# Optimization experiments

Measured on AMD Instinct MI355X. Metric: run time of the kernel, lower is better.

## Reference

```python
import jax, jax.numpy as jnp
import numpy as np


def _layernorm(x, g, b, eps=1e-5):
    mu = jnp.mean(x, axis=-1, keepdims=True)
    var = jnp.mean((x - mu) ** 2, axis=-1, keepdims=True)
    return g * (x - mu) * jax.lax.rsqrt(var + eps) + b


def _pos_encoding(S, D, dtype):
    # standard sinusoidal positional encoding [S, D]
    pos = jnp.arange(S, dtype=jnp.float32)[:, None]
    i = jnp.arange(0, D, 2, dtype=jnp.float32)[None, :]
    ang = pos / jnp.power(10000.0, i / D)
    return jnp.stack([jnp.sin(ang), jnp.cos(ang)], axis=-1).reshape(S, D).astype(dtype)


def _mha(x, theta, Wc, bc, num_heads):
    # Quantum projection: per-wire RX(x)+RX(theta) from |0>, <Z> = cos(x+theta).
    # The module uses ONE shared q_layer for q, k, v, so q == k == v.
    B, S, D = x.shape
    dk = D // num_heads
    p = jnp.cos(x + theta)                                    # [B,S,D]
    ph = p.reshape(B, S, num_heads, dk)                        # [B,S,H,dk]
    scale = 1.0 / jnp.sqrt(jnp.asarray(dk, x.dtype))
    scores = jnp.einsum('bqhd,bkhd->bhqk', ph, ph) * scale     # [B,H,S,S]
    attn = jax.nn.softmax(scores, axis=-1)
    out = jnp.einsum('bhqk,bkhd->bqhd', attn, ph).reshape(B, S, D)
    return out @ Wc + bc


def _ffn(x, theta, W1, b1, W2, b2):
    # RY-encoder + trainable RY per wire -> <Z> = cos(x + theta)
    h = jnp.cos(x + theta)
    h = h @ W1 + b1
    return jax.nn.relu(h) @ W2 + b2


def _forward(tokens, embedding, theta_attn, Wc, bc, ln1_g, ln1_b, theta_ffn,
             W1, b1, W2, b2, ln2_g, ln2_b, Wcls, bcls, num_heads):
    x = embedding[tokens]                                      # [B,S,D]
    B, S, D = x.shape
    x = x + _pos_encoding(S, D, x.dtype)
    n_blocks = theta_attn.shape[0]
    for l in range(n_blocks):  # small fixed layer count
        a = _mha(x, theta_attn[l], Wc[l], bc[l], num_heads)
        x = _layernorm(x + a, ln1_g[l], ln1_b[l])
        f = _ffn(x, theta_ffn[l], W1[l], b1[l], W2[l], b2[l])
        x = _layernorm(x + f, ln2_g[l], ln2_b[l])
    pooled = jnp.mean(x, axis=1)                               # [B,D]
    return pooled @ Wcls + bcls                                # [B,C]


def setup_inputs() -> dict:
    key = jax.random.key(0)
    ks = jax.random.split(key, 8)
    V, D, L, F, C = 32000, 512, 2, 2048, 10
    B, S = 8, 1024
    s = 0.02
    return {
        'tokens': jax.random.randint(ks[0], (B, S), 0, V, dtype=jnp.int32),
        'embedding': jax.random.normal(ks[1], (V, D), jnp.float32) * s,
        'theta_attn': jax.random.normal(ks[2], (L, D), jnp.float32) * s,
        'Wc': jax.random.normal(ks[3], (L, D, D), jnp.float32) * s,
        'bc': jnp.zeros((L, D), jnp.float32),
        'ln1_g': jnp.ones((L, D), jnp.float32),
        'ln1_b': jnp.zeros((L, D), jnp.float32),
        'theta_ffn': jax.random.normal(ks[4], (L, D), jnp.float32) * s,
        'W1': jax.random.normal(ks[5], (L, D, F), jnp.float32) * s,
        'b1': jnp.zeros((L, F), jnp.float32),
        'W2': jax.random.normal(ks[6], (L, F, D), jnp.float32) * s,
        'b2': jnp.zeros((L, D), jnp.float32),
        'ln2_g': jnp.ones((L, D), jnp.float32),
        'ln2_b': jnp.zeros((L, D), jnp.float32),
        'Wcls': jax.random.normal(ks[7], (D, C), jnp.float32) * s,
        'bcls': jnp.zeros((C,), jnp.float32),
        'num_heads': 8,
    }


def reference(tokens, embedding, theta_attn, Wc, bc, ln1_g, ln1_b, theta_ffn,
              W1, b1, W2, b2, ln2_g, ln2_b, Wcls, bcls, num_heads):
    return _forward(tokens, embedding, theta_attn, Wc, bc, ln1_g, ln1_b,
                    theta_ffn, W1, b1, W2, b2, ln2_g, ln2_b, Wcls, bcls, num_heads)
```

## Files before the change

### kernel.cpp

```cpp
#include <hip/hip_runtime.h>
#include <math.h>

#define BB 8
#define SS 1024
#define DD 512
#define HH 8
#define DK 64
#define FF 2048
#define NCLS 10
#define ROWS (BB*SS)
#define NLAYERS 2

typedef short bf16x8 __attribute__((ext_vector_type(8)));
typedef float f32x4 __attribute__((ext_vector_type(4)));

__device__ inline short f2bf(float f) {
    unsigned u = __float_as_uint(f);
    u += 0x7FFF + ((u >> 16) & 1);
    return (short)(u >> 16);
}

__device__ inline void gload_lds16(const void* g, void* l) {
    __builtin_amdgcn_global_load_lds((const __attribute__((address_space(1))) void*)g,
                                     (__attribute__((address_space(3))) void*)l, 16, 0, 0);
}

__global__ __launch_bounds__(128) void k_embed_pe(const int* __restrict__ tokens,
                                                  const float* __restrict__ emb,
                                                  float* __restrict__ x) {
    int row = blockIdx.x;
    int s = row & (SS - 1);
    int tok = tokens[row];
    const float4* e = reinterpret_cast<const float4*>(emb + (size_t)tok * DD);
    float4 v = e[threadIdx.x];
    float pe[4];
#pragma unroll
    for (int j = 0; j < 4; ++j) {
        int d = threadIdx.x * 4 + j;
        int jj = d >> 1;
        float inv = expf(-((float)(2 * jj) / (float)DD) * 9.210340371976184f);
        float ang = (float)s * inv;
        pe[j] = (d & 1) ? cosf(ang) : sinf(ang);
    }
    v.x += pe[0]; v.y += pe[1]; v.z += pe[2]; v.w += pe[3];
    reinterpret_cast<float4*>(x + (size_t)row * DD)[threadIdx.x] = v;
}

template <int WT>
__global__ __launch_bounds__(256) void k_cosp(const float* __restrict__ x,
                                              const float* __restrict__ theta,
                                              short* __restrict__ p,
                                              short* __restrict__ pt) {
    int d0 = blockIdx.x * 64, s0 = blockIdx.y * 64, b = blockIdx.z;
    int t = threadIdx.x;
    int tc = t & 15, tr = t >> 4;
    __shared__ short lt[64][68];
    float4 th = *reinterpret_cast<const float4*>(theta + d0 + tc * 4);
#pragma unroll
    for (int i = 0; i < 4; ++i) {
        int s = tr + 16 * i;
        float4 xv = *reinterpret_cast<const float4*>(
            x + ((size_t)b * SS + s0 + s) * DD + d0 + tc * 4);
        short4 o;
        o.x = f2bf(cosf(xv.x + th.x));
        o.y = f2bf(cosf(xv.y + th.y));
        o.z = f2bf(cosf(xv.z + th.z));
        o.w = f2bf(cosf(xv.w + th.w));
        *reinterpret_cast<short4*>(p + ((size_t)b * SS + s0 + s) * DD + d0 + tc * 4) = o;
        if (WT) {
            lt[tc * 4 + 0][s] = o.x;
            lt[tc * 4 + 1][s] = o.y;
            lt[tc * 4 + 2][s] = o.z;
            lt[tc * 4 + 3][s] = o.w;
        }
    }
    if (WT) {
        __syncthreads();
#pragma unroll
        for (int i = 0; i < 4; ++i) {
            int d = tr + 16 * i;
            short4 v;
            v.x = lt[d][tc * 4 + 0];
            v.y = lt[d][tc * 4 + 1];
            v.z = lt[d][tc * 4 + 2];
            v.w = lt[d][tc * 4 + 3];
            *reinterpret_cast<short4*>(pt + ((size_t)b * DD + d0 + d) * SS + s0 + tc * 4) = v;
        }
    }
}

__global__ __launch_bounds__(256) void k_wtrans(const float* __restrict__ W,
                                                short* __restrict__ Wt,
                                                int K, int N) {
    __shared__ float tile[32][33];
    int n0 = blockIdx.x * 32, k0 = blockIdx.y * 32;
    int tx = threadIdx.x & 31, ty = threadIdx.x >> 5;
#pragma unroll
    for (int i = 0; i < 4; ++i)
        tile[ty + 8 * i][tx] = W[(size_t)(k0 + ty + 8 * i) * N + n0 + tx];
    __syncthreads();
#pragma unroll
    for (int i = 0; i < 4; ++i)
        Wt[(size_t)(n0 + ty + 8 * i) * K + k0 + tx] = f2bf(tile[tx][ty + 8 * i]);
}

__global__ __launch_bounds__(256) void k_attn(const short* __restrict__ p,
                                              const short* __restrict__ pt,
                                              short* __restrict__ aout) {
    int qc = blockIdx.x, h = blockIdx.y, b = blockIdx.z;
    int t = threadIdx.x, w = t >> 6, l = t & 63;
    int lg = l >> 4, lr = l & 15;

    __shared__ __attribute__((aligned(16))) short Kt[128 * 64];
    __shared__ __attribute__((aligned(16))) short Vt[64 * 128];
    __shared__ __attribute__((aligned(16))) short Pl[4][16 * 136];

    const size_t prow = ((size_t)b * SS + qc * 64 + w * 16 + lr) * DD + h * DK;
    bf16x8 qf0 = *reinterpret_cast<const bf16x8*>(p + prow + lg * 8);
    bf16x8 qf1 = *reinterpret_cast<const bf16x8*>(p + prow + 32 + lg * 8);

    f32x4 acc[4];
#pragma unroll
    for (int dt = 0; dt < 4; ++dt) acc[dt] = (f32x4){0.f, 0.f, 0.f, 0.f};
    float denom = 0.f;

    const short* pK = p + (size_t)b * SS * DD + h * DK;
    const short* pV = pt + ((size_t)b * DD + h * DK) * SS;

    short* myP = &Pl[w][0];

    for (int k0 = 0; k0 < SS; k0 += 128) {
        __syncthreads();
#pragma unroll
        for (int i = 0; i < 4; ++i) {
            int c = i * 256 + t;
            int row = c >> 3, sl = c & 7, ssl = sl ^ (row & 7);
            gload_lds16(pK + (size_t)(k0 + row) * DD + ssl * 8,
                        Kt + (size_t)(i * 256 + w * 64) * 8);
        }
#pragma unroll
        for (int i = 0; i < 4; ++i) {
            int c = i * 256 + t;
            int row = c >> 4, sl = c & 15, ssl = sl ^ ((row & 7) * 2);
            gload_lds16(pV + (size_t)row * SS + k0 + ssl * 8,
                        Vt + (size_t)(i * 256 + w * 64) * 8);
        }
        asm volatile("s_waitcnt vmcnt(0)" ::: "memory");
        __syncthreads();

        f32x4 sc[8];
#pragma unroll
        for (int kt = 0; kt < 8; ++kt) {
            int row = kt * 16 + lr;
            bf16x8 ka0 = *reinterpret_cast<const bf16x8*>(Kt + row * 64 + ((lg ^ (row & 7)) * 8));
            bf16x8 ka1 = *reinterpret_cast<const bf16x8*>(Kt + row * 64 + (((lg + 4) ^ (row & 7)) * 8));
            f32x4 z = (f32x4){0.f, 0.f, 0.f, 0.f};
            z = __builtin_amdgcn_mfma_f32_16x16x32_bf16(ka0, qf0, z, 0, 0, 0);
            z = __builtin_amdgcn_mfma_f32_16x16x32_bf16(ka1, qf1, z, 0, 0, 0);
            sc[kt] = z;
        }
#pragma unroll
        for (int kt = 0; kt < 8; ++kt) {
            float e0 = __expf(sc[kt].x * 0.125f);
            float e1 = __expf(sc[kt].y * 0.125f);
            float e2 = __expf(sc[kt].z * 0.125f);
            float e3 = __expf(sc[kt].w * 0.125f);
            denom += (e0 + e1) + (e2 + e3);
            short4 pk;
            pk.x = f2bf(e0); pk.y = f2bf(e1); pk.z = f2bf(e2); pk.w = f2bf(e3);
            *reinterpret_cast<short4*>(myP + lr * 136 + kt * 16 + lg * 4) = pk;
        }
        asm volatile("s_waitcnt lgkmcnt(0)" ::: "memory");
#pragma unroll
        for (int kt2 = 0; kt2 < 4; ++kt2) {
            bf16x8 pb = *reinterpret_cast<const bf16x8*>(myP + lr * 136 + kt2 * 32 + lg * 8);
#pragma unroll
            for (int dt = 0; dt < 4; ++dt) {
                int row = dt * 16 + lr;
                bf16x8 va = *reinterpret_cast<const bf16x8*>(
                    Vt + row * 128 + (((kt2 * 4 + lg) ^ ((row & 7) * 2)) * 8));
                acc[dt] = __builtin_amdgcn_mfma_f32_16x16x32_bf16(va, pb, acc[dt], 0, 0, 0);
            }
        }
    }

    denom += __shfl_xor(denom, 16);
    denom += __shfl_xor(denom, 32);
    float inv = 1.0f / denom;

    size_t orow = ((size_t)b * SS + qc * 64 + w * 16 + lr) * DD + h * DK;
#pragma unroll
    for (int dt = 0; dt < 4; ++dt) {
        short4 o;
        o.x = f2bf(acc[dt].x * inv);
        o.y = f2bf(acc[dt].y * inv);
        o.z = f2bf(acc[dt].z * inv);
        o.w = f2bf(acc[dt].w * inv);
        *reinterpret_cast<short4*>(aout + orow + dt * 16 + lg * 4) = o;
    }
}

template <int RELU, int OUTBF>
__global__ __launch_bounds__(256) void k_mm(const short* __restrict__ A,
                                            const short* __restrict__ Bt,
                                            const float* __restrict__ bias,
                                            void* __restrict__ C,
                                            int N, int K) {
    __shared__ __attribute__((aligned(16))) short Al[128 * 32];
    __shared__ __attribute__((aligned(16))) short Bl[128 * 32];
    int t = threadIdx.x, w = t >> 6, l = t & 63;
    int lg = l >> 4, lr = l & 15;
    int wm = w >> 1, wn = w & 1;
    int row0 = blockIdx.y * 128, col0 = blockIdx.x * 128;

    f32x4 acc[4][4];
#pragma unroll
    for (int m = 0; m < 4; ++m)
#pragma unroll
        for (int n = 0; n < 4; ++n) acc[m][n] = (f32x4){0.f, 0.f, 0.f, 0.f};

    for (int k0 = 0; k0 < K; k0 += 32) {
        __syncthreads();
#pragma unroll
        for (int i = 0; i < 2; ++i) {
            int c = i * 256 + t;
            int row = c >> 2, sl = c & 3, ssl = sl ^ ((row >> 1) & 3);
            gload_lds16(A + (size_t)(row0 + row) * K + k0 + ssl * 8,
                        Al + (size_t)(i * 256 + w * 64) * 8);
            gload_lds16(Bt + (size_t)(col0 + row) * K + k0 + ssl * 8,
                        Bl + (size_t)(i * 256 + w * 64) * 8);
        }
        asm volatile("s_waitcnt vmcnt(0)" ::: "memory");
        __syncthreads();

        bf16x8 af[4], bfr[4];
#pragma unroll
        for (int m = 0; m < 4; ++m) {
            int row = wm * 64 + m * 16 + lr;
            af[m] = *reinterpret_cast<const bf16x8*>(Al + row * 32 + ((lg ^ ((row >> 1) & 3)) * 8));
        }
#pragma unroll
        for (int n = 0; n < 4; ++n) {
            int row = wn * 64 + n * 16 + lr;
            bfr[n] = *reinterpret_cast<const bf16x8*>(Bl + row * 32 + ((lg ^ ((row >> 1) & 3)) * 8));
        }
#pragma unroll
        for (int m = 0; m < 4; ++m)
#pragma unroll
            for (int n = 0; n < 4; ++n)
                acc[m][n] = __builtin_amdgcn_mfma_f32_16x16x32_bf16(af[m], bfr[n], acc[m][n], 0, 0, 0);
    }

    float bv[4];
#pragma unroll
    for (int n = 0; n < 4; ++n) bv[n] = bias[col0 + wn * 64 + n * 16 + lr];

#pragma unroll
    for (int m = 0; m < 4; ++m) {
#pragma unroll
        for (int n = 0; n < 4; ++n) {
            int col = col0 + wn * 64 + n * 16 + lr;
#pragma unroll
            for (int j = 0; j < 4; ++j) {
                int row = row0 + wm * 64 + m * 16 + lg * 4 + j;
                float v = acc[m][n][j] + bv[n];
                if (RELU) v = fmaxf(v, 0.f);
                if (OUTBF) ((short*)C)[(size_t)row * N + col] = f2bf(v);
                else       ((float*)C)[(size_t)row * N + col] = v;
            }
        }
    }
}

template <int COSP>
__global__ __launch_bounds__(128) void k_add_ln(float* __restrict__ x,
                                                const float* __restrict__ rr,
                                                const float* __restrict__ g,
                                                const float* __restrict__ bb,
                                                const float* __restrict__ theta,
                                                short* __restrict__ p) {
    int row = blockIdx.x;
    int t = threadIdx.x;
    float4 v = *reinterpret_cast<const float4*>(x + (size_t)row * DD + t * 4);
    float4 av = *reinterpret_cast<const float4*>(rr + (size_t)row * DD + t * 4);
    v.x += av.x; v.y += av.y; v.z += av.z; v.w += av.w;
    float s = v.x + v.y + v.z + v.w;
    float s2 = v.x * v.x + v.y * v.y + v.z * v.z + v.w * v.w;
#pragma unroll
    for (int off = 32; off > 0; off >>= 1) {
        s += __shfl_down(s, off);
        s2 += __shfl_down(s2, off);
    }
    __shared__ float ls[2], ls2[2];
    if ((t & 63) == 0) { ls[t >> 6] = s; ls2[t >> 6] = s2; }
    __syncthreads();
    float S1 = ls[0] + ls[1];
    float S2 = ls2[0] + ls2[1];
    float mu = S1 * (1.0f / DD);
    float var = S2 * (1.0f / DD) - mu * mu;
    float rstd = rsqrtf(var + 1e-5f);
    float4 gv = *reinterpret_cast<const float4*>(g + t * 4);
    float4 bv = *reinterpret_cast<const float4*>(bb + t * 4);
    float4 o;
    o.x = gv.x * (v.x - mu) * rstd + bv.x;
    o.y = gv.y * (v.y - mu) * rstd + bv.y;
    o.z = gv.z * (v.z - mu) * rstd + bv.z;
    o.w = gv.w * (v.w - mu) * rstd + bv.w;
    *reinterpret_cast<float4*>(x + (size_t)row * DD + t * 4) = o;
    if (COSP) {
        float4 th = *reinterpret_cast<const float4*>(theta + t * 4);
        short4 pk;
        pk.x = f2bf(cosf(o.x + th.x));
        pk.y = f2bf(cosf(o.y + th.y));
        pk.z = f2bf(cosf(o.z + th.z));
        pk.w = f2bf(cosf(o.w + th.w));
        *reinterpret_cast<short4*>(p + (size_t)row * DD + t * 4) = pk;
    }
}

__global__ __launch_bounds__(128) void k_pool(const float* __restrict__ x,
                                              float* __restrict__ part) {
    int b = blockIdx.x, c = blockIdx.y;
    int t = threadIdx.x;
    float4 s = {0.f, 0.f, 0.f, 0.f};
    for (int i = 0; i < 32; ++i) {
        float4 v = reinterpret_cast<const float4*>(
            x + ((size_t)b * SS + c * 32 + i) * DD)[t];
        s.x += v.x; s.y += v.y; s.z += v.z; s.w += v.w;
    }
    reinterpret_cast<float4*>(part + ((size_t)b * 32 + c) * DD)[t] = s;
}

__global__ __launch_bounds__(512) void k_cls(const float* __restrict__ part,
                                             const float* __restrict__ Wcls,
                                             const float* __restrict__ bcls,
                                             float* __restrict__ out) {
    int b = blockIdx.x;
    int t = threadIdx.x;
    float s = 0.f;
    for (int i = 0; i < 32; ++i) s += part[((size_t)b * 32 + i) * DD + t];
    float pooled = s * (1.0f / SS);
    float acc[NCLS];
#pragma unroll
    for (int c = 0; c < NCLS; ++c) acc[c] = pooled * Wcls[t * NCLS + c];
#pragma unroll
    for (int off = 32; off > 0; off >>= 1)
#pragma unroll
        for (int c = 0; c < NCLS; ++c) acc[c] += __shfl_xor(acc[c], off);
    __shared__ float wp[8][NCLS];
    int w = t >> 6, l = t & 63;
    if (l == 0)
#pragma unroll
        for (int c = 0; c < NCLS; ++c) wp[w][c] = acc[c];
    __syncthreads();
    if (t < NCLS) {
        float o = bcls[t];
#pragma unroll
        for (int i = 0; i < 8; ++i) o += wp[i][t];
        out[b * NCLS + t] = o;
    }
}

extern "C" void kernel_launch(void* const* d_in, const int* in_sizes, int n_in,
                              void* d_out, int out_size, void* d_ws, size_t ws_size,
                              hipStream_t stream) {
    const int* tokens      = (const int*)d_in[0];
    const float* emb       = (const float*)d_in[1];
    const float* theta_att = (const float*)d_in[2];
    const float* Wc        = (const float*)d_in[3];
    const float* bc        = (const float*)d_in[4];
    const float* ln1_g     = (const float*)d_in[5];
    const float* ln1_b     = (const float*)d_in[6];
    const float* theta_ffn = (const float*)d_in[7];
    const float* W1        = (const float*)d_in[8];
    const float* b1        = (const float*)d_in[9];
    const float* W2        = (const float*)d_in[10];
    const float* b2        = (const float*)d_in[11];
    const float* ln2_g     = (const float*)d_in[12];
    const float* ln2_b     = (const float*)d_in[13];
    const float* Wcls      = (const float*)d_in[14];
    const float* bcls      = (const float*)d_in[15];
    float* out = (float*)d_out;

    char* wsb = (char*)d_ws;
    float* x    = (float*)(wsb);
    float* t0   = (float*)(wsb + (size_t)16 * 1048576);
    short* p    = (short*)(wsb + (size_t)32 * 1048576);
    short* pt   = (short*)(wsb + (size_t)40 * 1048576);
    short* a    = (short*)(wsb + (size_t)48 * 1048576);
    short* hh   = (short*)(wsb + (size_t)56 * 1048576);
    short* Wct  = (short*)(wsb + (size_t)88 * 1048576);
    short* W1t  = (short*)(wsb + (size_t)89 * 1048576);
    short* W2t  = (short*)(wsb + (size_t)91 * 1048576);
    float* part = (float*)(wsb + (size_t)94 * 1048576);

    k_embed_pe<<<ROWS, 128, 0, stream>>>(tokens, emb, x);

    for (int l = 0; l < NLAYERS; ++l) {
        k_wtrans<<<dim3(DD / 32, DD / 32), 256, 0, stream>>>(Wc + (size_t)l * DD * DD, Wct, DD, DD);
        k_wtrans<<<dim3(FF / 32, DD / 32), 256, 0, stream>>>(W1 + (size_t)l * DD * FF, W1t, DD, FF);
        k_wtrans<<<dim3(DD / 32, FF / 32), 256, 0, stream>>>(W2 + (size_t)l * FF * DD, W2t, FF, DD);

        k_cosp<1><<<dim3(DD / 64, SS / 64, BB), 256, 0, stream>>>(x, theta_att + l * DD, p, pt);
        k_attn<<<dim3(SS / 64, HH, BB), 256, 0, stream>>>(p, pt, a);
        k_mm<0, 0><<<dim3(DD / 128, ROWS / 128), 256, 0, stream>>>(a, Wct, bc + l * DD, t0, DD, DD);
        k_add_ln<1><<<ROWS, 128, 0, stream>>>(x, t0, ln1_g + l * DD, ln1_b + l * DD,
                                              theta_ffn + l * DD, p);
        k_mm<1, 1><<<dim3(FF / 128, ROWS / 128), 256, 0, stream>>>(p, W1t, b1 + l * FF, hh, FF, DD);
        k_mm<0, 0><<<dim3(DD / 128, ROWS / 128), 256, 0, stream>>>(hh, W2t, b2 + l * DD, t0, DD, FF);
        k_add_ln<0><<<ROWS, 128, 0, stream>>>(x, t0, ln2_g + l * DD, ln2_b + l * DD,
                                              (const float*)nullptr, (short*)nullptr);
    }

    k_pool<<<dim3(BB, 32), 128, 0, stream>>>(x, part);
    k_cls<<<BB, 512, 0, stream>>>(part, Wcls, bcls, out);
}
```

Baseline: 478.9 us.

## Double-buffer GEMM LDS tiles and swizzle block order across XCDs

The GEMM kernel now uses two LDS buffers so the next K-tile's global-to-LDS loads are issued before the MFMAs on the current tile, overlapping memory latency with compute. The launch becomes a 1D grid, and block IDs are remapped with a modulo-8 interleave so neighbouring tiles land on the same XCD for better L2 reuse. LDS use doubles to 32KB per block, which may lower occupancy. A single barrier per iteration remains.

After: 463.5 us. 1.03x faster.

```diff
diff --git a/kernel.cpp b/kernel.cpp
--- a/kernel.cpp
+++ b/kernel.cpp
@@ -205,13 +205,18 @@
                                             const short* __restrict__ Bt,
                                             const float* __restrict__ bias,
                                             void* __restrict__ C,
-                                            int N, int K) {
-    __shared__ __attribute__((aligned(16))) short Al[128 * 32];
-    __shared__ __attribute__((aligned(16))) short Bl[128 * 32];
+                                            int N, int K, int gx) {
+    __shared__ __attribute__((aligned(16))) short Al[2][128 * 32];
+    __shared__ __attribute__((aligned(16))) short Bl[2][128 * 32];
     int t = threadIdx.x, w = t >> 6, l = t & 63;
     int lg = l >> 4, lr = l & 15;
     int wm = w >> 1, wn = w & 1;
-    int row0 = blockIdx.y * 128, col0 = blockIdx.x * 128;
+
+    int nwg = gridDim.x;
+    int bid = blockIdx.x;
+    int swz = (bid & 7) * (nwg >> 3) + (bid >> 3);
+    int bx = swz % gx, by = swz / gx;
+    int row0 = by * 128, col0 = bx * 128;
 
     f32x4 acc[4][4];
 #pragma unroll
@@ -219,37 +224,54 @@
 #pragma unroll
         for (int n = 0; n < 4; ++n) acc[m][n] = (f32x4){0.f, 0.f, 0.f, 0.f};
 
-    for (int k0 = 0; k0 < K; k0 += 32) {
-        __syncthreads();
-#pragma unroll
-        for (int i = 0; i < 2; ++i) {
-            int c = i * 256 + t;
-            int row = c >> 2, sl = c & 3, ssl = sl ^ ((row >> 1) & 3);
-            gload_lds16(A + (size_t)(row0 + row) * K + k0 + ssl * 8,
-                        Al + (size_t)(i * 256 + w * 64) * 8);
-            gload_lds16(Bt + (size_t)(col0 + row) * K + k0 + ssl * 8,
-                        Bl + (size_t)(i * 256 + w * 64) * 8);
-        }
-        asm volatile("s_waitcnt vmcnt(0)" ::: "memory");
-        __syncthreads();
-
+#define STAGE_MM(buf, kk0)                                                      \
+    {                                                                           \
+        _Pragma("unroll")                                                       \
+        for (int i = 0; i < 2; ++i) {                                           \
+            int c = i * 256 + t;                                                \
+            int row = c >> 2, sl = c & 3, ssl = sl ^ ((row >> 1) & 3);          \
+            gload_lds16(A + (size_t)(row0 + row) * K + (kk0) + ssl * 8,         \
+                        &Al[buf][0] + (size_t)(i * 256 + w * 64) * 8);          \
+            gload_lds16(Bt + (size_t)(col0 + row) * K + (kk0) + ssl * 8,        \
+                        &Bl[buf][0] + (size_t)(i * 256 + w * 64) * 8);          \
+        }                                                                       \
+    }
+
+    STAGE_MM(0, 0);
+    asm volatile("s_waitcnt vmcnt(0)" ::: "memory");
+    __syncthreads();
+
+    const int nk = K >> 5;
+    int cur = 0;
+    for (int kt = 0; kt < nk; ++kt) {
+        if (kt + 1 < nk) STAGE_MM(cur ^ 1, (kt + 1) * 32);
+
+        const short* a_ = &Al[cur][0];
+        const short* b_ = &Bl[cur][0];
         bf16x8 af[4], bfr[4];
 #pragma unroll
         for (int m = 0; m < 4; ++m) {
             int row = wm * 64 + m * 16 + lr;
-            af[m] = *reinterpret_cast<const bf16x8*>(Al + row * 32 + ((lg ^ ((row >> 1) & 3)) * 8));
+            af[m] = *reinterpret_cast<const bf16x8*>(a_ + row * 32 + ((lg ^ ((row >> 1) & 3)) * 8));
         }
 #pragma unroll
         for (int n = 0; n < 4; ++n) {
             int row = wn * 64 + n * 16 + lr;
-            bfr[n] = *reinterpret_cast<const bf16x8*>(Bl + row * 32 + ((lg ^ ((row >> 1) & 3)) * 8));
+            bfr[n] = *reinterpret_cast<const bf16x8*>(b_ + row * 32 + ((lg ^ ((row >> 1) & 3)) * 8));
         }
 #pragma unroll
         for (int m = 0; m < 4; ++m)
 #pragma unroll
             for (int n = 0; n < 4; ++n)
                 acc[m][n] = __builtin_amdgcn_mfma_f32_16x16x32_bf16(af[m], bfr[n], acc[m][n], 0, 0, 0);
-    }
+
+        if (kt + 1 < nk) {
+            asm volatile("s_waitcnt vmcnt(0)" ::: "memory");
+            __syncthreads();
+            cur ^= 1;
+        }
+    }
+#undef STAGE_MM
 
     float bv[4];
 #pragma unroll
@@ -403,11 +425,14 @@
 
         k_cosp<1><<<dim3(DD / 64, SS / 64, BB), 256, 0, stream>>>(x, theta_att + l * DD, p, pt);
         k_attn<<<dim3(SS / 64, HH, BB), 256, 0, stream>>>(p, pt, a);
-        k_mm<0, 0><<<dim3(DD / 128, ROWS / 128), 256, 0, stream>>>(a, Wct, bc + l * DD, t0, DD, DD);
+        k_mm<0, 0><<<(DD / 128) * (ROWS / 128), 256, 0, stream>>>(
+            a, Wct, bc + l * DD, t0, DD, DD, DD / 128);
         k_add_ln<1><<<ROWS, 128, 0, stream>>>(x, t0, ln1_g + l * DD, ln1_b + l * DD,
                                               theta_ffn + l * DD, p);
-        k_mm<1, 1><<<dim3(FF / 128, ROWS / 128), 256, 0, stream>>>(p, W1t, b1 + l * FF, hh, FF, DD);
-        k_mm<0, 0><<<dim3(DD / 128, ROWS / 128), 256, 0, stream>>>(hh, W2t, b2 + l * DD, t0, DD, FF);
+        k_mm<1, 1><<<(FF / 128) * (ROWS / 128), 256, 0, stream>>>(
+            p, W1t, b1 + l * FF, hh, FF, DD, FF / 128);
+        k_mm<0, 0><<<(DD / 128) * (ROWS / 128), 256, 0, stream>>>(
+            hh, W2t, b2 + l * DD, t0, DD, FF, DD / 128);
         k_add_ln<0><<<ROWS, 128, 0, stream>>>(x, t0, ln2_g + l * DD, ln2_b + l * DD,
                                               (const float*)nullptr, (short*)nullptr);
     }
```
